# Kernel optimization log

Hardware: AMD Instinct MI355X
Metric: run time of the kernel (lower is better)

## Reference

```python
import jax, jax.numpy as jnp
import numpy as np

D_MODEL = 1024
HEADS = 16
DK = D_MODEL // HEADS
LAYERS = 4
BATCH = 8
SEQ = 1024
EPS = 1e-5


def _ln2(x):
    # torch LayerNorm([seq_len, d_model]) with default (untrained) affine: gamma=1, beta=0
    m = jnp.mean(x, axis=(1, 2), keepdims=True)
    v = jnp.var(x, axis=(1, 2), keepdims=True)
    return (x - m) * jax.lax.rsqrt(v + EPS)


def _pos_enc(seq_len, d_model):
    pos = jnp.arange(seq_len, dtype=jnp.float32)[:, None]
    i = jnp.arange(d_model)
    angle = pos / jnp.power(1000.0, (2 * (i // 2)).astype(jnp.float32) / d_model)
    return jnp.where(i % 2 == 0, jnp.sin(angle), jnp.cos(angle))  # [S, D]


def setup_inputs() -> dict:
    key = jax.random.key(0)
    ks = jax.random.split(key, 12)
    s = 0.02
    X = jax.random.normal(ks[0], (BATCH, SEQ, D_MODEL), dtype=jnp.float32)
    Wq = jax.random.normal(ks[1], (LAYERS, HEADS, DK, D_MODEL), dtype=jnp.float32) * s
    Wk = jax.random.normal(ks[2], (LAYERS, HEADS, DK, D_MODEL), dtype=jnp.float32) * s
    Wv = jax.random.normal(ks[3], (LAYERS, HEADS, DK, D_MODEL), dtype=jnp.float32) * s
    W0 = jax.random.normal(ks[4], (LAYERS, D_MODEL, D_MODEL), dtype=jnp.float32) * s
    Wr_w = jax.random.normal(ks[5], (LAYERS, D_MODEL, D_MODEL), dtype=jnp.float32) * s
    Wr_b = jax.random.normal(ks[6], (LAYERS, D_MODEL), dtype=jnp.float32) * s
    Wf0_w = jax.random.normal(ks[7], (LAYERS, D_MODEL, D_MODEL), dtype=jnp.float32) * s
    Wf0_b = jax.random.normal(ks[8], (LAYERS, D_MODEL), dtype=jnp.float32) * s
    Wf1_w = jax.random.normal(ks[9], (LAYERS, D_MODEL, D_MODEL), dtype=jnp.float32) * s
    Wf1_b = jax.random.normal(ks[10], (LAYERS, D_MODEL), dtype=jnp.float32) * s
    return {"X": X, "Wq": Wq, "Wk": Wk, "Wv": Wv, "W0": W0,
            "Wr_w": Wr_w, "Wr_b": Wr_b, "Wf0_w": Wf0_w, "Wf0_b": Wf0_b,
            "Wf1_w": Wf1_w, "Wf1_b": Wf1_b}


def reference(X, Wq, Wk, Wv, W0, Wr_w, Wr_b, Wf0_w, Wf0_b, Wf1_w, Wf1_b):
    B, S, D = X.shape
    x = X + _pos_enc(S, D)[None]
    scale = 1.0 / jnp.sqrt(jnp.float32(DK))
    for l in range(LAYERS):
        # batched multi-head projections (equivalent to per-head Linear + concat)
        Q = jnp.einsum('bsd,hkd->bhsk', x, Wq[l])
        K = jnp.einsum('bsd,hkd->bhsk', x, Wk[l])
        V = jnp.einsum('bsd,hkd->bhsk', x, Wv[l])
        scores = jnp.einsum('bhsk,bhtk->bhst', Q, K) * scale
        A = jax.nn.softmax(scores, axis=-1)
        O = jnp.einsum('bhst,bhtk->bhsk', A, V)
        O = O.transpose(0, 2, 1, 3).reshape(B, S, D)  # concat heads on feature dim
        mha = O @ W0[l].T
        r0 = _ln2(x + mha) @ Wr_w[l].T + Wr_b[l]
        ff = jax.nn.relu(r0 @ Wf0_w[l].T + Wf0_b[l]) @ Wf1_w[l].T + Wf1_b[l]
        x = _ln2(ff + r0) @ Wr_w[l].T + Wr_b[l]
    return x
```

## Files before the change

kernel.cpp:

```cpp
#include <hip/hip_runtime.h>
#include <hip/hip_bf16.h>
#include <math.h>

#define D_MODEL 1024
#define HEADS   16
#define DKV     64
#define LAYERS  4
#define BATCH   8
#define SEQ     1024
#define NTOK    (BATCH*SEQ)
#define LN_N    (SEQ*D_MODEL)
#define EPSV    1e-5f

typedef __attribute__((ext_vector_type(8))) short short8;
typedef __attribute__((ext_vector_type(4))) float floatx4;

__device__ __forceinline__ float bf2f(ushort u) {
    union { uint i; float f; } v; v.i = ((uint)u) << 16; return v.f;
}
__device__ __forceinline__ ushort f2bf(float f) {
    union { float f; uint i; } v; v.f = f;
    uint r = (v.i + 0x7fffu + ((v.i >> 16) & 1u)) >> 16;
    return (ushort)r;
}
__device__ __forceinline__ uint cvtpk(float a, float b) {
    uint r;
    asm("v_cvt_pk_bf16_f32 %0, %1, %2" : "=v"(r) : "v"(a), "v"(b));
    return r;
}
__device__ __forceinline__ void pl32(uint &a, uint &c) {
    asm volatile("v_permlane32_swap_b32 %0, %1" : "+v"(a), "+v"(c));
}
__device__ __forceinline__ void pl16(uint &a, uint &c) {
    asm volatile("v_permlane16_swap_b32 %0, %1" : "+v"(a), "+v"(c));
}

__device__ __forceinline__ void gload16(const ushort* g, ushort* l) {
    __builtin_amdgcn_global_load_lds(
        (const __attribute__((address_space(1))) void*)g,
        (__attribute__((address_space(3))) void*)l, 16, 0, 0);
}

template<int BK>
__device__ __forceinline__ void gemm_coreT(
    const ushort* __restrict__ A, const ushort* __restrict__ B,
    int lda, int ldb, int Kd,
    ushort* ldsA, ushort* ldsB, floatx4 (&acc)[4][4])
{
    constexpr int CH = BK / 8;
    constexpr int TB = 128 * BK;
    const int tid  = threadIdx.x;
    const int lane = tid & 63;
    const int w    = tid >> 6;
    const int wm   = w >> 1, wn = w & 1;
    const int mn   = lane & 15, quad = lane >> 4;

    auto stage = [&](int k0, int buf) {
#pragma unroll
        for (int s = 0; s < CH / 2; s++) {
            int lin = s * 256 + tid;
            int r   = lin / CH;
            int cp  = lin % CH;
            int cs_ = cp ^ (r & (CH - 1));
            gload16(A + (size_t)r * lda + k0 + cs_ * 8, ldsA + buf * TB + lin * 8);
            gload16(B + (size_t)r * ldb + k0 + cs_ * 8, ldsB + buf * TB + lin * 8);
        }
    };

    stage(0, 0);
    __syncthreads();

    int cur = 0;
    for (int k0 = 0; k0 < Kd; k0 += BK) {
        if (k0 + BK < Kd) stage(k0 + BK, cur ^ 1);
        const ushort* cA = ldsA + cur * TB;
        const ushort* cB = ldsB + cur * TB;
#pragma unroll
        for (int kk = 0; kk < BK / 32; kk++) {
            short8 af[4], bfr[4];
#pragma unroll
            for (int i = 0; i < 4; i++) {
                int r = wm * 64 + i * 16 + mn;
                int c = (kk * 4 + quad) ^ (r & (CH - 1));
                af[i] = *(const short8*)(cA + r * BK + c * 8);
            }
#pragma unroll
            for (int j = 0; j < 4; j++) {
                int r = wn * 64 + j * 16 + mn;
                int c = (kk * 4 + quad) ^ (r & (CH - 1));
                bfr[j] = *(const short8*)(cB + r * BK + c * 8);
            }
#pragma unroll
            for (int i = 0; i < 4; i++)
#pragma unroll
                for (int j = 0; j < 4; j++)
                    acc[i][j] = __builtin_amdgcn_mfma_f32_16x16x32_bf16(af[i], bfr[j], acc[i][j], 0, 0, 0);
        }
        __syncthreads();
        cur ^= 1;
    }
}

__global__ __launch_bounds__(256) void gemm_bt128(
    const ushort* __restrict__ A, const ushort* __restrict__ B,
    const float* __restrict__ bias, ushort* __restrict__ C,
    const ushort* __restrict__ resid, float* __restrict__ statsOut,
    float* __restrict__ outF, int relu,
    const float* __restrict__ lnIn, const float* __restrict__ csum)
{
    __shared__ ushort ldsA[2 * 128 * 64], ldsB[2 * 128 * 64];
    __shared__ float sred1[4], sred2[4];
    const int lid = blockIdx.y * 64 + blockIdx.x;
    const int xcd = lid & 7, idx = lid >> 3;
    const int bx = xcd * 8 + (idx >> 3);
    const int by = idx & 7;
    floatx4 acc[4][4];
#pragma unroll
    for (int i = 0; i < 4; i++)
#pragma unroll
        for (int j = 0; j < 4; j++) acc[i][j] = (floatx4){0.f, 0.f, 0.f, 0.f};

    gemm_coreT<64>(A + (size_t)bx * 128 * D_MODEL,
                   B + (size_t)by * 128 * D_MODEL,
                   D_MODEL, D_MODEL, D_MODEL, ldsA, ldsB, acc);

    const int lane = threadIdx.x & 63, w = threadIdx.x >> 6;
    const int wm = w >> 1, wn = w & 1;
    const int mn = lane & 15, quad = lane >> 4;
    const int bsmp = bx >> 3;
    float mean = 0.f, rln = 1.f;
    if (lnIn) {
        float sum = lnIn[bsmp], sq = lnIn[32 + bsmp];
        mean = sum * (1.f / (float)LN_N);
        rln  = rsqrtf(sq * (1.f / (float)LN_N) - mean * mean + EPSV);
    }
    float ssum = 0.f, ssq = 0.f;
#pragma unroll
    for (int i = 0; i < 4; i++) {
#pragma unroll
        for (int j = 0; j < 4; j++) {
            int col = by * 128 + wn * 64 + j * 16 + mn;
            float bv = bias ? bias[col] : 0.f;
            float cj = csum ? csum[col] : 0.f;
#pragma unroll
            for (int r = 0; r < 4; r++) {
                int row = bx * 128 + wm * 64 + i * 16 + quad * 4 + r;
                float v = acc[i][j][r];
                if (lnIn) v = (v - mean * cj) * rln;
                v += bv;
                if (relu) v = fmaxf(v, 0.f);
                if (resid) {
                    v += bf2f(resid[(size_t)row * D_MODEL + col]);
                    ssum += v; ssq += v * v;
                }
                if (outF) outF[(size_t)row * D_MODEL + col] = v;
                else      C[(size_t)row * D_MODEL + col] = f2bf(v);
            }
        }
    }
    if (statsOut) {
        for (int o = 1; o < 64; o <<= 1) {
            ssum += __shfl_xor(ssum, o); ssq += __shfl_xor(ssq, o);
        }
        if (lane == 0) { sred1[w] = ssum; sred2[w] = ssq; }
        __syncthreads();
        if (threadIdx.x == 0) {
            atomicAdd(&statsOut[bsmp],      sred1[0] + sred1[1] + sred1[2] + sred1[3]);
            atomicAdd(&statsOut[32 + bsmp], sred2[0] + sred2[1] + sred2[2] + sred2[3]);
        }
    }
}

__global__ __launch_bounds__(256) void gemm_qkv(
    const ushort* __restrict__ X, const ushort* __restrict__ Wq,
    const ushort* __restrict__ Wk, const ushort* __restrict__ Wv,
    ushort* __restrict__ Q, ushort* __restrict__ K, ushort* __restrict__ Vt)
{
    __shared__ ushort ldsA[2 * 128 * 32], ldsB[2 * 128 * 32];
    const int lid = blockIdx.y * 64 + blockIdx.x;
    const int xcd = lid & 7, idx = lid >> 3;
    const int bx = xcd * 8 + idx / 24;
    const int byy = idx % 24;
    const int which = byy >> 3;
    const int nb = byy & 7;
    const ushort* B = (which == 0) ? Wq : (which == 1) ? Wk : Wv;
    floatx4 acc[4][4];
#pragma unroll
    for (int i = 0; i < 4; i++)
#pragma unroll
        for (int j = 0; j < 4; j++) acc[i][j] = (floatx4){0.f, 0.f, 0.f, 0.f};

    gemm_coreT<32>(X + (size_t)bx * 128 * D_MODEL,
                   B + (size_t)nb * 128 * D_MODEL,
                   D_MODEL, D_MODEL, D_MODEL, ldsA, ldsB, acc);

    const int lane = threadIdx.x & 63, w = threadIdx.x >> 6;
    const int wm = w >> 1, wn = w & 1;
    const int mn = lane & 15, quad = lane >> 4;
    if (which == 2) {
#pragma unroll
        for (int i = 0; i < 4; i++) {
#pragma unroll
            for (int j = 0; j < 4; j++) {
                int col = nb * 128 + wn * 64 + j * 16 + mn;
                int h = col >> 6, kk = col & 63;
                int row0 = bx * 128 + wm * 64 + i * 16 + quad * 4;
                int b = row0 >> 10, t0 = row0 & 1023;
                uint2 uu;
                uu.x = cvtpk(acc[i][j][0], acc[i][j][1]);
                uu.y = cvtpk(acc[i][j][2], acc[i][j][3]);
                *(uint2*)(Vt + (((size_t)(b * HEADS + h)) * DKV + kk) * SEQ + t0) = uu;
            }
        }
    } else {
        ushort* dst = (which == 0) ? Q : K;
        const float scl = (which == 0) ? 0.125f : 1.0f;
#pragma unroll
        for (int i = 0; i < 4; i++) {
#pragma unroll
            for (int j = 0; j < 4; j++) {
                int col = nb * 128 + wn * 64 + j * 16 + mn;
#pragma unroll
                for (int r = 0; r < 4; r++) {
                    int row = bx * 128 + wm * 64 + i * 16 + quad * 4 + r;
                    dst[(size_t)row * D_MODEL + col] = f2bf(acc[i][j][r] * scl);
                }
            }
        }
    }
}

__global__ __launch_bounds__(256) void flash_attn(
    const ushort* __restrict__ Q, const ushort* __restrict__ K,
    const ushort* __restrict__ Vt, ushort* __restrict__ O)
{
    __shared__ ushort lK[64 * 128];
    __shared__ ushort lV[64 * 128];
    const int tid = threadIdx.x, lane = tid & 63, w = tid >> 6;
    const int mn = lane & 15, quad = lane >> 4;
    const int pair = blockIdx.x;
    const int qt = blockIdx.y;
    const int b = pair >> 4, h = pair & 15;
    const ushort* Qb = Q + ((size_t)b * SEQ) * D_MODEL + h * DKV;
    const ushort* Kb = K + ((size_t)b * SEQ) * D_MODEL + h * DKV;
    const ushort* Vb = Vt + (size_t)pair * DKV * SEQ;

    short8 bq[2][2];
#pragma unroll
    for (int i = 0; i < 2; i++)
#pragma unroll
        for (int kk = 0; kk < 2; kk++)
            bq[i][kk] = *(const short8*)(Qb +
                (size_t)(qt * 128 + w * 32 + i * 16 + mn) * D_MODEL + kk * 32 + quad * 8);

    auto stage_K = [&](int tkk) {
#pragma unroll
        for (int c = 0; c < 4; c++) {
            int lin = c * 256 + tid;
            int rw = lin >> 4;
            int cc0 = (lin & 15) ^ (rw & 7);
            int r = rw + ((cc0 >> 3) << 6);
            gload16(Kb + (size_t)(tkk * 128 + r) * D_MODEL + (cc0 & 7) * 8,
                    lK + lin * 8);
        }
    };
    auto stage_V = [&](int tkk) {
#pragma unroll
        for (int c = 0; c < 4; c++) {
            int lin = c * 256 + tid;
            int rw = lin >> 4;
            int cc0 = (lin & 15) ^ (rw & 7);
            gload16(Vb + (size_t)rw * SEQ + tkk * 128 + cc0 * 8,
                    lV + lin * 8);
        }
    };

    stage_K(0); stage_V(0);
    __syncthreads();

    floatx4 acc_o[2][4];
    float lrow[2] = {0.f, 0.f};
#pragma unroll
    for (int i = 0; i < 2; i++)
#pragma unroll
        for (int jo = 0; jo < 4; jo++) acc_o[i][jo] = (floatx4){0.f, 0.f, 0.f, 0.f};

    for (int tk = 0; tk < 8; tk++) {
        floatx4 s[2][8];
#pragma unroll
        for (int i = 0; i < 2; i++)
#pragma unroll
            for (int j = 0; j < 8; j++) s[i][j] = (floatx4){0.f, 0.f, 0.f, 0.f};
        __builtin_amdgcn_s_setprio(1);
#pragma unroll
        for (int kk = 0; kk < 2; kk++) {
#pragma unroll
            for (int j = 0; j < 8; j++) {
                int krow = (j & 3) * 16 + mn;
                int kch = (((j >> 2) * 8 + kk * 4 + quad) ^ (mn & 7));
                short8 ak = *(const short8*)(lK + krow * 128 + kch * 8);
                s[0][j] = __builtin_amdgcn_mfma_f32_16x16x32_bf16(ak, bq[0][kk], s[0][j], 0, 0, 0);
                s[1][j] = __builtin_amdgcn_mfma_f32_16x16x32_bf16(ak, bq[1][kk], s[1][j], 0, 0, 0);
            }
        }
        __builtin_amdgcn_s_setprio(0);
        __syncthreads();
        if (tk < 7) stage_K(tk + 1);

        uint pw[2][8][2];
#pragma unroll
        for (int i = 0; i < 2; i++) {
            float ps = 0.f;
#pragma unroll
            for (int j = 0; j < 8; j++) {
                float p0 = __expf(s[i][j][0]), p1 = __expf(s[i][j][1]);
                float p2 = __expf(s[i][j][2]), p3 = __expf(s[i][j][3]);
                ps += (p0 + p1) + (p2 + p3);
                pw[i][j][0] = cvtpk(p0, p1);
                pw[i][j][1] = cvtpk(p2, p3);
            }
            ps += __shfl_xor(ps, 16);
            ps += __shfl_xor(ps, 32);
            lrow[i] += ps;
        }

        __builtin_amdgcn_s_setprio(1);
#pragma unroll
        for (int kk = 0; kk < 4; kk++) {
            union { short8 s8; uint u[4]; } pa[2];
#pragma unroll
            for (int i = 0; i < 2; i++) {
                uint A = pw[i][2 * kk][0],     Bw = pw[i][2 * kk][1];
                uint C = pw[i][2 * kk + 1][0], D  = pw[i][2 * kk + 1][1];
                pl32(A, C);  pl16(A, C);
                pl32(Bw, D); pl16(Bw, D);
                pa[i].u[0] = A; pa[i].u[1] = Bw; pa[i].u[2] = C; pa[i].u[3] = D;
            }
#pragma unroll
            for (int jo = 0; jo < 4; jo++) {
                int vch = ((kk * 4 + quad) ^ (mn & 7));
                short8 bv = *(const short8*)(lV + (jo * 16 + mn) * 128 + vch * 8);
                acc_o[0][jo] = __builtin_amdgcn_mfma_f32_16x16x32_bf16(pa[0].s8, bv, acc_o[0][jo], 0, 0, 0);
                acc_o[1][jo] = __builtin_amdgcn_mfma_f32_16x16x32_bf16(pa[1].s8, bv, acc_o[1][jo], 0, 0, 0);
            }
        }
        __builtin_amdgcn_s_setprio(0);
        __syncthreads();
        if (tk < 7) stage_V(tk + 1);
    }

#pragma unroll
    for (int i = 0; i < 2; i++)
#pragma unroll
        for (int r = 0; r < 4; r++) {
            float rs = __shfl(lrow[i], quad * 4 + r);
            float rinv = 1.f / rs;
            int row = qt * 128 + w * 32 + i * 16 + quad * 4 + r;
#pragma unroll
            for (int jo = 0; jo < 4; jo++)
                O[((size_t)b * SEQ + row) * D_MODEL + h * DKV + jo * 16 + mn] =
                    f2bf(acc_o[i][jo][r] * rinv);
        }
}

__global__ __launch_bounds__(256) void cvt_f32_bf16(const float* __restrict__ src,
                                                    ushort* __restrict__ dst) {
    size_t base = ((size_t)blockIdx.x * 256 + threadIdx.x) * 8;
    float4 a = *(const float4*)(src + base);
    float4 b = *(const float4*)(src + base + 4);
    short8 o;
    o[0] = (short)f2bf(a.x); o[1] = (short)f2bf(a.y);
    o[2] = (short)f2bf(a.z); o[3] = (short)f2bf(a.w);
    o[4] = (short)f2bf(b.x); o[5] = (short)f2bf(b.y);
    o[6] = (short)f2bf(b.z); o[7] = (short)f2bf(b.w);
    *(short8*)(dst + base) = o;
}

__global__ __launch_bounds__(256) void add_pos(const float* __restrict__ X,
                                               ushort* __restrict__ x) {
    size_t idx = (size_t)blockIdx.x * 256 + threadIdx.x;
    int d = (int)(idx & (D_MODEL - 1));
    int s = (int)((idx >> 10) & (SEQ - 1));
    float freq = powf(1000.f, (float)(2 * (d >> 1)) * (1.f / (float)D_MODEL));
    float ang = (float)s / freq;
    float pe = (d & 1) ? cosf(ang) : sinf(ang);
    x[idx] = f2bf(X[idx] + pe);
}

__global__ __launch_bounds__(256) void colsum_k(const ushort* __restrict__ W,
                                                float* __restrict__ cs) {
    int row = blockIdx.x * 4 + (threadIdx.x >> 6);
    int lane = threadIdx.x & 63;
    const ushort* Wr = W + (size_t)row * D_MODEL;
    float s = 0.f;
#pragma unroll
    for (int p = 0; p < 2; p++) {
        short8 v = *(const short8*)(Wr + p * 512 + lane * 8);
#pragma unroll
        for (int e = 0; e < 8; e++) s += bf2f((ushort)v[e]);
    }
#pragma unroll
    for (int o = 1; o < 64; o <<= 1) s += __shfl_xor(s, o);
    if (lane == 0) cs[row] = s;
}

__global__ void zero_stats512(float* stats) {
    stats[threadIdx.x] = 0.f; stats[256 + threadIdx.x] = 0.f;
}

extern "C" void kernel_launch(void* const* d_in, const int* in_sizes, int n_in,
                              void* d_out, int out_size, void* d_ws, size_t ws_size,
                              hipStream_t stream) {
    const float* X    = (const float*)d_in[0];
    const float* Wq   = (const float*)d_in[1];
    const float* Wk   = (const float*)d_in[2];
    const float* Wv   = (const float*)d_in[3];
    const float* W0   = (const float*)d_in[4];
    const float* Wr_w = (const float*)d_in[5];
    const float* Wr_b = (const float*)d_in[6];
    const float* Wf0w = (const float*)d_in[7];
    const float* Wf0b = (const float*)d_in[8];
    const float* Wf1w = (const float*)d_in[9];
    const float* Wf1b = (const float*)d_in[10];
    float* out = (float*)d_out;

    char* ws = (char*)d_ws;
    size_t off = 0;
    auto alloc = [&](size_t bytes) -> void* {
        void* p = ws + off; off += (bytes + 255) & ~(size_t)255; return p;
    };
    const size_t ACT = (size_t)NTOK * D_MODEL * sizeof(ushort);
    const size_t WTE = (size_t)LAYERS * D_MODEL * D_MODEL;
    ushort* x  = (ushort*)alloc(ACT);
    ushort* bQ = (ushort*)alloc(ACT);
    ushort* bK = (ushort*)alloc(ACT);
    ushort* bV = (ushort*)alloc(ACT);
    ushort* bO = (ushort*)alloc(ACT);
    ushort* wq  = (ushort*)alloc(WTE * 2);
    ushort* wk  = (ushort*)alloc(WTE * 2);
    ushort* wv  = (ushort*)alloc(WTE * 2);
    ushort* w0  = (ushort*)alloc(WTE * 2);
    ushort* wr  = (ushort*)alloc(WTE * 2);
    ushort* wf0 = (ushort*)alloc(WTE * 2);
    ushort* wf1 = (ushort*)alloc(WTE * 2);
    float* stats = (float*)alloc(8 * 64 * sizeof(float));
    float* csr   = (float*)alloc(WTE / D_MODEL * sizeof(float));

    const int CVT_BLOCKS = (int)(WTE / (256 * 8));
    const dim3 GEMM_GRID(NTOK / 128, D_MODEL / 128);
    const dim3 QKV_GRID(NTOK / 128, 3 * D_MODEL / 128);
    const dim3 FLASH_GRID(BATCH * HEADS, SEQ / 128);

    cvt_f32_bf16<<<CVT_BLOCKS, 256, 0, stream>>>(Wq,   wq);
    cvt_f32_bf16<<<CVT_BLOCKS, 256, 0, stream>>>(Wk,   wk);
    cvt_f32_bf16<<<CVT_BLOCKS, 256, 0, stream>>>(Wv,   wv);
    cvt_f32_bf16<<<CVT_BLOCKS, 256, 0, stream>>>(W0,   w0);
    cvt_f32_bf16<<<CVT_BLOCKS, 256, 0, stream>>>(Wr_w, wr);
    cvt_f32_bf16<<<CVT_BLOCKS, 256, 0, stream>>>(Wf0w, wf0);
    cvt_f32_bf16<<<CVT_BLOCKS, 256, 0, stream>>>(Wf1w, wf1);
    colsum_k<<<LAYERS * D_MODEL / 4, 256, 0, stream>>>(wr, csr);
    zero_stats512<<<1, 256, 0, stream>>>(stats);

    add_pos<<<(NTOK * D_MODEL) / 256, 256, 0, stream>>>(X, x);

    for (int l = 0; l < LAYERS; l++) {
        const size_t WO = (size_t)l * D_MODEL * D_MODEL;
        const ushort* Wq_l  = wq  + WO;
        const ushort* Wk_l  = wk  + WO;
        const ushort* Wv_l  = wv  + WO;
        const ushort* W0_l  = w0  + WO;
        const ushort* Wr_l  = wr  + WO;
        const ushort* W0w_l = wf0 + WO;
        const ushort* W1w_l = wf1 + WO;
        const float* Wrb_l = Wr_b + (size_t)l * D_MODEL;
        const float* W0b_l = Wf0b + (size_t)l * D_MODEL;
        const float* W1b_l = Wf1b + (size_t)l * D_MODEL;
        const float* cs_l  = csr + (size_t)l * D_MODEL;
        float* st0 = stats + (size_t)(2 * l) * 64;
        float* st1 = stats + (size_t)(2 * l + 1) * 64;

        gemm_qkv<<<QKV_GRID, 256, 0, stream>>>(x, Wq_l, Wk_l, Wv_l, bQ, bK, bV);

        flash_attn<<<FLASH_GRID, 256, 0, stream>>>(bQ, bK, bV, bO);

        gemm_bt128<<<GEMM_GRID, 256, 0, stream>>>(bO, W0_l, nullptr, bK,
            x, st0, nullptr, 0, nullptr, nullptr);
        gemm_bt128<<<GEMM_GRID, 256, 0, stream>>>(bK, Wr_l, Wrb_l, bV,
            nullptr, nullptr, nullptr, 0, st0, cs_l);
        gemm_bt128<<<GEMM_GRID, 256, 0, stream>>>(bV, W0w_l, W0b_l, bQ,
            nullptr, nullptr, nullptr, 1, nullptr, nullptr);
        gemm_bt128<<<GEMM_GRID, 256, 0, stream>>>(bQ, W1w_l, W1b_l, bO,
            bV, st1, nullptr, 0, nullptr, nullptr);
        gemm_bt128<<<GEMM_GRID, 256, 0, stream>>>(bO, Wr_l, Wrb_l, x,
            nullptr, nullptr, (l == LAYERS - 1) ? out : nullptr, 0, st1, cs_l);
    }
}
```

Measured before the change: 1.335 ms.

## Replace double-buffered GEMM core with 4-stage async LDS pipeline

Replaces the templated double-buffered GEMM mainloop with a 4-buffer BK=32 pipeline that keeps three global-to-LDS loads in flight. It uses explicit vmcnt waits, a single barrier per k-step, and s_setprio around the MFMA block. The swizzle also changes to XOR on row pairs. The aim is to hide global load latency and cut barrier stalls in the projection and QKV GEMMs. The cost is fixed LDS use and correctness that depends on hand-counted vmcnt values and a single barrier protecting buffer reuse.

```diff
diff --git a/kernel.cpp b/kernel.cpp
--- a/kernel.cpp
+++ b/kernel.cpp
@@ -41,63 +41,64 @@
         (__attribute__((address_space(3))) void*)l, 16, 0, 0);
 }
 
-template<int BK>
-__device__ __forceinline__ void gemm_coreT(
+#define TB32 (128*32)
+__device__ __forceinline__ void gemm_core_p4(
     const ushort* __restrict__ A, const ushort* __restrict__ B,
-    int lda, int ldb, int Kd,
+    int lda, int ldb,
     ushort* ldsA, ushort* ldsB, floatx4 (&acc)[4][4])
 {
-    constexpr int CH = BK / 8;
-    constexpr int TB = 128 * BK;
-    const int tid  = threadIdx.x;
-    const int lane = tid & 63;
-    const int w    = tid >> 6;
-    const int wm   = w >> 1, wn = w & 1;
-    const int mn   = lane & 15, quad = lane >> 4;
-
-    auto stage = [&](int k0, int buf) {
-#pragma unroll
-        for (int s = 0; s < CH / 2; s++) {
-            int lin = s * 256 + tid;
-            int r   = lin / CH;
-            int cp  = lin % CH;
-            int cs_ = cp ^ (r & (CH - 1));
-            gload16(A + (size_t)r * lda + k0 + cs_ * 8, ldsA + buf * TB + lin * 8);
-            gload16(B + (size_t)r * ldb + k0 + cs_ * 8, ldsB + buf * TB + lin * 8);
-        }
+    constexpr int NK = D_MODEL / 32;
+    const int tid = threadIdx.x, lane = tid & 63, w = tid >> 6;
+    const int wm = w >> 1, wn = w & 1;
+    const int mn = lane & 15, quad = lane >> 4;
+
+    const int r0 = tid >> 2, cp0 = tid & 3;
+    const int csrc = (cp0 ^ ((r0 >> 1) & 3)) * 8;
+    const ushort* gA0 = A + (size_t)r0 * lda + csrc;
+    const ushort* gA1 = gA0 + (size_t)64 * lda;
+    const ushort* gB0 = B + (size_t)r0 * ldb + csrc;
+    const ushort* gB1 = gB0 + (size_t)64 * ldb;
+    ushort* lA0 = ldsA + tid * 8;
+    ushort* lB0 = ldsB + tid * 8;
+
+    auto stage = [&](int t) {
+        const int bo = (t & 3) * TB32;
+        const int k0 = t * 32;
+        gload16(gA0 + k0, lA0 + bo);
+        gload16(gA1 + k0, lA0 + bo + 2048);
+        gload16(gB0 + k0, lB0 + bo);
+        gload16(gB1 + k0, lB0 + bo + 2048);
     };
 
-    stage(0, 0);
-    __syncthreads();
-
-    int cur = 0;
-    for (int k0 = 0; k0 < Kd; k0 += BK) {
-        if (k0 + BK < Kd) stage(k0 + BK, cur ^ 1);
-        const ushort* cA = ldsA + cur * TB;
-        const ushort* cB = ldsB + cur * TB;
-#pragma unroll
-        for (int kk = 0; kk < BK / 32; kk++) {
-            short8 af[4], bfr[4];
-#pragma unroll
-            for (int i = 0; i < 4; i++) {
-                int r = wm * 64 + i * 16 + mn;
-                int c = (kk * 4 + quad) ^ (r & (CH - 1));
-                af[i] = *(const short8*)(cA + r * BK + c * 8);
-            }
-#pragma unroll
-            for (int j = 0; j < 4; j++) {
-                int r = wn * 64 + j * 16 + mn;
-                int c = (kk * 4 + quad) ^ (r & (CH - 1));
-                bfr[j] = *(const short8*)(cB + r * BK + c * 8);
-            }
-#pragma unroll
-            for (int i = 0; i < 4; i++)
-#pragma unroll
-                for (int j = 0; j < 4; j++)
-                    acc[i][j] = __builtin_amdgcn_mfma_f32_16x16x32_bf16(af[i], bfr[j], acc[i][j], 0, 0, 0);
-        }
-        __syncthreads();
-        cur ^= 1;
+    stage(0); stage(1); stage(2);
+
+    const int crd = (quad ^ ((mn >> 1) & 3)) * 8;
+
+#pragma unroll 1
+    for (int t = 0; t < NK; ++t) {
+        if (t < NK - 2)       asm volatile("s_waitcnt vmcnt(8)" ::: "memory");
+        else if (t == NK - 2) asm volatile("s_waitcnt vmcnt(4)" ::: "memory");
+        else                  asm volatile("s_waitcnt vmcnt(0)" ::: "memory");
+        __builtin_amdgcn_s_barrier();
+        __builtin_amdgcn_sched_barrier(0);
+        if (t + 3 < NK) stage(t + 3);
+        __builtin_amdgcn_sched_barrier(0);
+        const ushort* cA = ldsA + (t & 3) * TB32;
+        const ushort* cB = ldsB + (t & 3) * TB32;
+        short8 af[4], bfr[4];
+#pragma unroll
+        for (int i = 0; i < 4; i++)
+            af[i] = *(const short8*)(cA + (wm * 64 + i * 16 + mn) * 32 + crd);
+#pragma unroll
+        for (int j = 0; j < 4; j++)
+            bfr[j] = *(const short8*)(cB + (wn * 64 + j * 16 + mn) * 32 + crd);
+        __builtin_amdgcn_s_setprio(1);
+#pragma unroll
+        for (int i = 0; i < 4; i++)
+#pragma unroll
+            for (int j = 0; j < 4; j++)
+                acc[i][j] = __builtin_amdgcn_mfma_f32_16x16x32_bf16(af[i], bfr[j], acc[i][j], 0, 0, 0);
+        __builtin_amdgcn_s_setprio(0);
     }
 }
 
@@ -108,7 +109,7 @@
     float* __restrict__ outF, int relu,
     const float* __restrict__ lnIn, const float* __restrict__ csum)
 {
-    __shared__ ushort ldsA[2 * 128 * 64], ldsB[2 * 128 * 64];
+    __shared__ ushort ldsA[4 * TB32], ldsB[4 * TB32];
     __shared__ float sred1[4], sred2[4];
     const int lid = blockIdx.y * 64 + blockIdx.x;
     const int xcd = lid & 7, idx = lid >> 3;
@@ -120,9 +121,9 @@
 #pragma unroll
         for (int j = 0; j < 4; j++) acc[i][j] = (floatx4){0.f, 0.f, 0.f, 0.f};
 
-    gemm_coreT<64>(A + (size_t)bx * 128 * D_MODEL,
-                   B + (size_t)by * 128 * D_MODEL,
-                   D_MODEL, D_MODEL, D_MODEL, ldsA, ldsB, acc);
+    gemm_core_p4(A + (size_t)bx * 128 * D_MODEL,
+                 B + (size_t)by * 128 * D_MODEL,
+                 D_MODEL, D_MODEL, ldsA, ldsB, acc);
 
     const int lane = threadIdx.x & 63, w = threadIdx.x >> 6;
     const int wm = w >> 1, wn = w & 1;
@@ -176,7 +177,7 @@
     const ushort* __restrict__ Wk, const ushort* __restrict__ Wv,
     ushort* __restrict__ Q, ushort* __restrict__ K, ushort* __restrict__ Vt)
 {
-    __shared__ ushort ldsA[2 * 128 * 32], ldsB[2 * 128 * 32];
+    __shared__ ushort ldsA[4 * TB32], ldsB[4 * TB32];
     const int lid = blockIdx.y * 64 + blockIdx.x;
     const int xcd = lid & 7, idx = lid >> 3;
     const int bx = xcd * 8 + idx / 24;
@@ -190,9 +191,9 @@
 #pragma unroll
         for (int j = 0; j < 4; j++) acc[i][j] = (floatx4){0.f, 0.f, 0.f, 0.f};
 
-    gemm_coreT<32>(X + (size_t)bx * 128 * D_MODEL,
-                   B + (size_t)nb * 128 * D_MODEL,
-                   D_MODEL, D_MODEL, D_MODEL, ldsA, ldsB, acc);
+    gemm_core_p4(X + (size_t)bx * 128 * D_MODEL,
+                 B + (size_t)nb * 128 * D_MODEL,
+                 D_MODEL, D_MODEL, ldsA, ldsB, acc);
 
     const int lane = threadIdx.x & 63, w = threadIdx.x >> 6;
     const int wm = w >> 1, wn = w & 1;
```

Measured after the change: 1.465 ms. 1.1x slower.
